# Kernel optimization log

Measured on AMD Instinct MI355X. Metric: run time of the kernel, lower is better.

Reference implementation:

```python
import jax, jax.numpy as jnp
import numpy as np

B, N = 1, 512
C_S, C_Z, C_H, H, PQ, PV = 384, 128, 16, 12, 4, 8
INF, EPS = 1e5, 1e-8
HW_INIT = 0.541324854612918  # softplus^{-1}(1), ipa_point_weights_init_


def _rotary(t, rot_dim, theta=10000.0):
    # lucidrains interleaved rotary over residue axis (axis 1); rotates first rot_dim channels
    n = t.shape[1]
    inv_freq = 1.0 / (theta ** (jnp.arange(0, rot_dim, 2, dtype=jnp.float32) / rot_dim))
    freqs = jnp.arange(n, dtype=jnp.float32)[:, None] * inv_freq  # [N, rot_dim//2]
    cos = jnp.cos(freqs)[None, :, None, :].astype(t.dtype)
    sin = jnp.sin(freqs)[None, :, None, :].astype(t.dtype)
    tr, tp = t[..., :rot_dim], t[..., rot_dim:]
    x1, x2 = tr[..., 0::2], tr[..., 1::2]
    tr = jnp.stack([x1 * cos - x2 * sin, x1 * sin + x2 * cos], axis=-1).reshape(tr.shape)
    return jnp.concatenate([tr, tp], axis=-1)


def _ipa(s, z, rot, trans, mask, Wq, bq, Wkv, bkv, Wqp, bqp, Wkvp, bkvp, Wb, bb,
         head_weights, Whid, bhid, Wpair, bpair, Wpts, bpts, Wpn, bpn):
    Bx, Nx = s.shape[0], s.shape[1]
    q = (s @ Wq + bq).reshape(Bx, Nx, H, C_H)
    kv = (s @ Wkv + bkv).reshape(Bx, Nx, H, 2 * C_H)
    k, v = kv[..., :C_H], kv[..., C_H:]

    def make_pts(x, npts):
        # channel layout: [x-block, y-block, z-block] -> [B,N,H*npts,3], then rigid apply R@p+t
        x = jnp.stack(jnp.split(x, 3, axis=-1), axis=-1)
        x = jnp.einsum('bnij,bnpj->bnpi', rot, x) + trans[:, :, None, :]
        return x.reshape(Bx, Nx, H, npts, 3)

    q_pts = make_pts(s @ Wqp + bqp, PQ)
    kv_pts = make_pts(s @ Wkvp + bkvp, PQ + PV)
    k_pts, v_pts = kv_pts[..., :PQ, :], kv_pts[..., PQ:, :]

    q = _rotary(q, C_H // 2)
    k = _rotary(k, C_H // 2)

    a = jnp.einsum('bihc,bjhc->bhij', q, k) * np.sqrt(1.0 / (3 * C_H))
    a = a + np.sqrt(1.0 / 3.0) * (jnp.einsum('bijc,ch->bhij', z, Wb) + bb[None, :, None, None])
    d2 = jnp.sum((q_pts[:, :, None] - k_pts[:, None]) ** 2, axis=-1)  # [B,Ni,Nj,H,PQ]
    hw = jax.nn.softplus(head_weights) * np.sqrt(1.0 / (3 * (PQ * 9.0 / 2)))
    a = a + jnp.transpose(-0.5 * jnp.sum(d2 * hw[None, None, None, :, None], axis=-1), (0, 3, 1, 2))
    sq_mask = INF * (mask[:, :, None] * mask[:, None, :] - 1.0)
    a = jax.nn.softmax(a + sq_mask[:, None], axis=-1)  # [B,H,N,N]

    o = jnp.einsum('bhij,bjhc->bihc', a, v).reshape(Bx, Nx, H * C_H)
    o_pt = jnp.einsum('bhij,bjhpx->bihpx', a, v_pts)  # [B,N,H,PV,3]
    o_pt = jnp.einsum('bnji,bnhpj->bnhpi', rot, o_pt - trans[:, :, None, None, :])  # invert_apply
    o_pt_norm = jnp.sqrt(jnp.sum(o_pt ** 2, axis=-1) + EPS).reshape(Bx, Nx, H * PV)
    o_pt = o_pt.reshape(Bx, Nx, H * PV, 3)
    pts_feat = jnp.concatenate([o_pt[..., 0], o_pt[..., 1], o_pt[..., 2]], axis=-1)
    o_pair = jnp.einsum('bhij,bijc->bihc', a, z).reshape(Bx, Nx, H * C_Z)

    s_out = ((o @ Whid + bhid) + (o_pair @ Wpair + bpair)
             + (pts_feat @ Wpts + bpts) + (o_pt_norm @ Wpn + bpn))
    return s_out, a


def setup_inputs() -> dict:
    key = jax.random.key(0)
    ks = jax.random.split(key, 16)
    f = lambda i, shape: jax.random.normal(ks[i], shape, dtype=jnp.float32)
    sc = 0.02
    rot, _ = jnp.linalg.qr(f(2, (B, N, 3, 3)))
    return {
        's': f(0, (B, N, C_S)),
        'z': f(1, (B, N, N, C_Z)),
        'rot': rot,
        'trans': f(3, (B, N, 3)),
        'mask': jnp.ones((B, N), jnp.float32),
        'Wq': f(4, (C_S, H * C_H)) * sc, 'bq': jnp.zeros((H * C_H,), jnp.float32),
        'Wkv': f(5, (C_S, 2 * H * C_H)) * sc, 'bkv': jnp.zeros((2 * H * C_H,), jnp.float32),
        'Wqp': f(6, (C_S, H * PQ * 3)) * sc, 'bqp': jnp.zeros((H * PQ * 3,), jnp.float32),
        'Wkvp': f(7, (C_S, H * (PQ + PV) * 3)) * sc, 'bkvp': jnp.zeros((H * (PQ + PV) * 3,), jnp.float32),
        'Wb': f(8, (C_Z, H)) * sc, 'bb': jnp.zeros((H,), jnp.float32),
        'head_weights': jnp.full((H,), HW_INIT, jnp.float32),
        'Whid': f(9, (H * C_H, C_S)) * sc, 'bhid': jnp.zeros((C_S,), jnp.float32),
        'Wpair': f(10, (H * C_Z, C_S)) * sc, 'bpair': jnp.zeros((C_S,), jnp.float32),
        'Wpts': f(11, (H * PV * 3, C_S)) * sc, 'bpts': jnp.zeros((C_S,), jnp.float32),
        'Wpn': f(12, (H * PV, C_S)) * sc, 'bpn': jnp.zeros((C_S,), jnp.float32),
    }


def reference(s, z, rot, trans, mask, Wq, bq, Wkv, bkv, Wqp, bqp, Wkvp, bkvp, Wb, bb,
              head_weights, Whid, bhid, Wpair, bpair, Wpts, bpts, Wpn, bpn):
    return _ipa(s, z, rot, trans, mask, Wq, bq, Wkv, bkv, Wqp, bqp, Wkvp, bkvp, Wb, bb,
                head_weights, Whid, bhid, Wpair, bpair, Wpts, bpts, Wpn, bpn)
```

## Files before the change

kernel.cpp:

```cpp
#include <hip/hip_runtime.h>
#include <hip/hip_bf16.h>
#include <cmath>

#define N 512
#define C_S 384
#define C_Z 128
#define C_H 16
#define H 12
#define PQ 4
#define PV 8

#define NJC 4
#define JCHUNK (N / NJC)
#define NPART 2016
#define NFEAT 2112
#define NRAW 1152
#define KSPLIT 11
#define KCHUNK 192

#define WS_Q    0
#define WS_K    (WS_Q + N*H*C_H)
#define WS_V    (WS_K + N*H*C_H)
#define WS_QP   (WS_V + N*H*C_H)
#define WS_KP   (WS_QP + N*H*PQ*3)
#define WS_VP   (WS_KP + N*H*PQ*3)
#define WS_PART (WS_VP + N*H*PV*3)
#define WS_FEAT (WS_PART + N*NJC*NPART)
#define WS_RAW  WS_PART
#define WS_KT   (WS_PART + 1200000)
#define WS_KPT  (WS_KT + 98304)
#define WS_WBT  (WS_KPT + 73728)
#define WS_FOUT WS_PART

__global__ __launch_bounds__(256) void k_gemm_proj(
    const float* __restrict__ s,
    const float* __restrict__ Wq,  const float* __restrict__ bq,
    const float* __restrict__ Wkv, const float* __restrict__ bkv,
    const float* __restrict__ Wqp, const float* __restrict__ bqp,
    const float* __restrict__ Wkvp,const float* __restrict__ bkvp,
    float* __restrict__ raw_out)
{
    const int m0 = blockIdx.x * 64;
    const int c0 = blockIdx.y * 64;
    const int t  = threadIdx.x;
    const int tc = t & 15;
    const int tm = t >> 4;

    __shared__ float st[64 * 33];
    __shared__ float wt[32 * 64];

    float acc[4][4];
#pragma unroll
    for (int u = 0; u < 4; ++u) {
        int col = c0 + tc*4 + u;
        const float* b; int cb;
        if (col < 192)      { b = bq;   cb = 0; }
        else if (col < 576) { b = bkv;  cb = 192; }
        else if (col < 720) { b = bqp;  cb = 576; }
        else                { b = bkvp; cb = 720; }
        float bv = b[col - cb];
#pragma unroll
        for (int r = 0; r < 4; ++r) acc[r][u] = bv;
    }

    for (int k0 = 0; k0 < C_S; k0 += 32) {
        __syncthreads();
        for (int e = t; e < 512; e += 256) {
            int row = e >> 3, kq = e & 7;
            float4 v = *(const float4*)&s[(size_t)(m0 + row)*C_S + k0 + kq*4];
            st[row*33 + kq*4 + 0] = v.x;
            st[row*33 + kq*4 + 1] = v.y;
            st[row*33 + kq*4 + 2] = v.z;
            st[row*33 + kq*4 + 3] = v.w;
        }
        for (int e = t; e < 512; e += 256) {
            int kk = e >> 4, c4 = e & 15;
            int col = c0 + c4*4;
            const float* W; int ncol, cb;
            if (col < 192)      { W = Wq;   ncol = 192; cb = 0; }
            else if (col < 576) { W = Wkv;  ncol = 384; cb = 192; }
            else if (col < 720) { W = Wqp;  ncol = 144; cb = 576; }
            else                { W = Wkvp; ncol = 432; cb = 720; }
            float4 v = *(const float4*)&W[(size_t)(k0 + kk)*ncol + (col - cb)];
            *(float4*)&wt[kk*64 + c4*4] = v;
        }
        __syncthreads();

#pragma unroll 8
        for (int kk = 0; kk < 32; ++kk) {
            float4 w = *(const float4*)&wt[kk*64 + tc*4];
            float sv[4];
#pragma unroll
            for (int r = 0; r < 4; ++r) sv[r] = st[(tm*4 + r)*33 + kk];
#pragma unroll
            for (int r = 0; r < 4; ++r) {
                acc[r][0] += sv[r] * w.x;
                acc[r][1] += sv[r] * w.y;
                acc[r][2] += sv[r] * w.z;
                acc[r][3] += sv[r] * w.w;
            }
        }
    }

#pragma unroll
    for (int r = 0; r < 4; ++r) {
        float4 o = make_float4(acc[r][0], acc[r][1], acc[r][2], acc[r][3]);
        *(float4*)&raw_out[(size_t)(m0 + tm*4 + r)*NRAW + c0 + tc*4] = o;
    }
}

__global__ __launch_bounds__(256) void k_post(
    const float* __restrict__ raw_in, const float* __restrict__ rot,
    const float* __restrict__ trans, const float* __restrict__ Wb,
    float* __restrict__ ws)
{
    const int n = blockIdx.x;
    const int t = threadIdx.x;
    __shared__ float raw[NRAW];

    for (int idx = t; idx < NRAW; idx += 256) raw[idx] = raw_in[(size_t)n*NRAW + idx];
    __syncthreads();

    if (n == 0) {
        for (int idx = t; idx < H*C_Z; idx += 256) {
            int h = idx >> 7, c = idx & 127;
            ws[WS_WBT + h*128 + c] = Wb[c*H + h];
        }
    }

    float R[9], T[3];
#pragma unroll
    for (int u = 0; u < 9; ++u) R[u] = rot[n*9 + u];
#pragma unroll
    for (int u = 0; u < 3; ++u) T[u] = trans[n*3 + u];

    float* q   = ws + WS_Q;
    float* v   = ws + WS_V;
    float* qp  = ws + WS_QP;
    float* vp  = ws + WS_VP;
    float* kT  = ws + WS_KT;
    float* kpT = ws + WS_KPT;

    for (int idx = t; idx < 1152; idx += 256) {
        if (idx < 192) {
            int h = idx >> 4, c = idx & 15;
            float val;
            if (c < 8) {
                int f = c >> 1;
                float x1 = raw[h*16 + 2*f];
                float x2 = raw[h*16 + 2*f + 1];
                float ang = (float)n * powf(10000.0f, -(float)(2*f) / 8.0f);
                float cs = cosf(ang), sn = sinf(ang);
                val = (c & 1) ? (x1*sn + x2*cs) : (x1*cs - x2*sn);
            } else {
                val = raw[h*16 + c];
            }
            q[n*192 + idx] = val;
        } else if (idx < 384) {
            int o = idx - 192, h = o >> 4, c = o & 15;
            float val;
            if (c < 8) {
                int f = c >> 1;
                float x1 = raw[192 + h*32 + 2*f];
                float x2 = raw[192 + h*32 + 2*f + 1];
                float ang = (float)n * powf(10000.0f, -(float)(2*f) / 8.0f);
                float cs = cosf(ang), sn = sinf(ang);
                val = (c & 1) ? (x1*sn + x2*cs) : (x1*cs - x2*sn);
            } else {
                val = raw[192 + h*32 + c];
            }
            kT[(size_t)o*N + n] = val;
        } else if (idx < 576) {
            int o = idx - 384, h = o >> 4, c = o & 15;
            v[n*192 + o] = raw[192 + h*32 + 16 + c];
        } else if (idx < 720) {
            int o = idx - 576;
            int hp = o / 3, ic = o - hp*3;
            float acc = T[ic];
#pragma unroll
            for (int j = 0; j < 3; ++j) acc += R[ic*3 + j] * raw[576 + j*48 + hp];
            qp[n*144 + o] = acc;
        } else {
            int o = idx - 720;
            int hp = o / 3, ic = o - hp*3;
            int h = hp / 12, p = hp - h*12;
            float acc = T[ic];
#pragma unroll
            for (int j = 0; j < 3; ++j) acc += R[ic*3 + j] * raw[720 + j*144 + hp];
            if (p < PQ) kpT[(size_t)(h*12 + p*3 + ic)*N + n] = acc;
            else        vp[n*(H*PV*3) + (h*PV + (p - PQ))*3 + ic] = acc;
        }
    }
}

__global__ __launch_bounds__(256) void k_logits(
    const float* __restrict__ ws, const float* __restrict__ z,
    const float* __restrict__ bb,
    const float* __restrict__ hwts, const float* __restrict__ mask,
    float* __restrict__ a_out)
{
    const int i  = blockIdx.x;
    const int j0 = blockIdx.y * 64;
    const int t  = threadIdx.x;
    const int j  = t & 63;
    const int jg = j0 + j;
    const int h0 = __builtin_amdgcn_readfirstlane(3 * (t >> 6));

    __shared__ float zt[64*132];

    const int srow = t >> 2;
    const int scq  = t & 3;
    float4 ra0, ra1, ra2, ra3, rb0, rb1, rb2, rb3;
    {
        const float* zbase = z + (((size_t)i*N) + j0)*C_Z;
        int e0 = t,       r0_ = e0 >> 4, c0_ = e0 & 15;
        int e1 = t + 256, r1_ = e1 >> 4, c1_ = e1 & 15;
        int e2 = t + 512, r2_ = e2 >> 4, c2_ = e2 & 15;
        int e3 = t + 768, r3_ = e3 >> 4, c3_ = e3 & 15;
        ra0 = *(const float4*)&zbase[(size_t)r0_*C_Z + c0_*4];
        ra1 = *(const float4*)&zbase[(size_t)r1_*C_Z + c1_*4];
        ra2 = *(const float4*)&zbase[(size_t)r2_*C_Z + c2_*4];
        ra3 = *(const float4*)&zbase[(size_t)r3_*C_Z + c3_*4];
        rb0 = *(const float4*)&zbase[(size_t)r0_*C_Z + 64 + c0_*4];
        rb1 = *(const float4*)&zbase[(size_t)r1_*C_Z + 64 + c1_*4];
        rb2 = *(const float4*)&zbase[(size_t)r2_*C_Z + 64 + c2_*4];
        rb3 = *(const float4*)&zbase[(size_t)r3_*C_Z + 64 + c3_*4];
    }

    const float* q   = ws + WS_Q  + (size_t)i*192;
    const float* qp  = ws + WS_QP + (size_t)i*144;
    const float* kT  = ws + WS_KT;
    const float* kpT = ws + WS_KPT;

    const float c1 = sqrtf(1.0f / 48.0f);
    const float c2 = sqrtf(1.0f / 3.0f);
    const float mterm = 100000.0f * (mask[i] * mask[jg] - 1.0f);

    float qkd[3];
#pragma unroll
    for (int u = 0; u < 3; ++u) {
        const int h = h0 + u;
        float qk = 0.0f;
#pragma unroll
        for (int c = 0; c < 16; ++c)
            qk += q[h*16 + c] * kT[(size_t)(h*16 + c)*N + jg];
        float d2s = 0.0f;
#pragma unroll
        for (int e = 0; e < 12; ++e) {
            float d = qp[h*12 + e] - kpT[(size_t)(h*12 + e)*N + jg];
            d2s += d*d;
        }
        float hw = log1pf(expf(hwts[h])) * sqrtf(1.0f / 54.0f);
        qkd[u] = c1*qk - 0.5f*hw*d2s + mterm + c2*bb[h];
    }

    {
        int e0 = t,       r0_ = e0 >> 4, c0_ = e0 & 15;
        int e1 = t + 256, r1_ = e1 >> 4, c1_ = e1 & 15;
        int e2 = t + 512, r2_ = e2 >> 4, c2_ = e2 & 15;
        int e3 = t + 768, r3_ = e3 >> 4, c3_ = e3 & 15;
        *(float4*)&zt[r0_*132 + c0_*4] = ra0;
        *(float4*)&zt[r1_*132 + c1_*4] = ra1;
        *(float4*)&zt[r2_*132 + c2_*4] = ra2;
        *(float4*)&zt[r3_*132 + c3_*4] = ra3;
    }
    __syncthreads();

    const float* w0 = ws + WS_WBT + (size_t)h0*128;
    float acc[3] = {0.0f, 0.0f, 0.0f};
#pragma unroll
    for (int c4 = 0; c4 < 16; ++c4) {
        float4 zv = *(const float4*)&zt[j*132 + c4*4];
        float4 b0 = *(const float4*)&w0[c4*4];
        float4 b1 = *(const float4*)&w0[128 + c4*4];
        float4 b2 = *(const float4*)&w0[256 + c4*4];
        acc[0] += zv.x*b0.x + zv.y*b0.y + zv.z*b0.z + zv.w*b0.w;
        acc[1] += zv.x*b1.x + zv.y*b1.y + zv.z*b1.z + zv.w*b1.w;
        acc[2] += zv.x*b2.x + zv.y*b2.y + zv.z*b2.z + zv.w*b2.w;
    }
    __syncthreads();

    {
        int e0 = t,       r0_ = e0 >> 4, c0_ = e0 & 15;
        int e1 = t + 256, r1_ = e1 >> 4, c1_ = e1 & 15;
        int e2 = t + 512, r2_ = e2 >> 4, c2_ = e2 & 15;
        int e3 = t + 768, r3_ = e3 >> 4, c3_ = e3 & 15;
        *(float4*)&zt[r0_*132 + 64 + c0_*4] = rb0;
        *(float4*)&zt[r1_*132 + 64 + c1_*4] = rb1;
        *(float4*)&zt[r2_*132 + 64 + c2_*4] = rb2;
        *(float4*)&zt[r3_*132 + 64 + c3_*4] = rb3;
    }
    __syncthreads();

#pragma unroll
    for (int c4 = 16; c4 < 32; ++c4) {
        float4 zv = *(const float4*)&zt[j*132 + c4*4];
        float4 b0 = *(const float4*)&w0[c4*4];
        float4 b1 = *(const float4*)&w0[128 + c4*4];
        float4 b2 = *(const float4*)&w0[256 + c4*4];
        acc[0] += zv.x*b0.x + zv.y*b0.y + zv.z*b0.z + zv.w*b0.w;
        acc[1] += zv.x*b1.x + zv.y*b1.y + zv.z*b1.z + zv.w*b1.w;
        acc[2] += zv.x*b2.x + zv.y*b2.y + zv.z*b2.z + zv.w*b2.w;
    }

#pragma unroll
    for (int u = 0; u < 3; ++u)
        a_out[((size_t)(h0 + u)*N + i)*N + jg] = qkd[u] + c2*acc[u];
}

__global__ __launch_bounds__(256) void k_softmax(float* __restrict__ a)
{
    const int row  = blockIdx.x*4 + (threadIdx.x >> 6);
    const int lane = threadIdx.x & 63;
    float* r = a + (size_t)row * N;

    float v[8];
    float m = -1e30f;
#pragma unroll
    for (int u = 0; u < 8; ++u) { v[u] = r[lane + 64*u]; m = fmaxf(m, v[u]); }
#pragma unroll
    for (int off = 32; off; off >>= 1) m = fmaxf(m, __shfl_xor(m, off));
    float ssum = 0.0f;
#pragma unroll
    for (int u = 0; u < 8; ++u) { v[u] = expf(v[u] - m); ssum += v[u]; }
#pragma unroll
    for (int off = 32; off; off >>= 1) ssum += __shfl_xor(ssum, off);
    float inv = 1.0f / ssum;
#pragma unroll
    for (int u = 0; u < 8; ++u) r[lane + 64*u] = v[u] * inv;
}

__global__ __launch_bounds__(256) void k_av(
    const float* __restrict__ a_full, const float* __restrict__ ws_ro,
    const float* __restrict__ z, float* __restrict__ ws)
{
    const int i  = blockIdx.x;
    const int jc = blockIdx.y;
    const int j0 = jc * JCHUNK;
    const int t  = threadIdx.x;

    __shared__ float a_s[H*JCHUNK];

    const float* v  = ws_ro + WS_V;
    const float* vp = ws_ro + WS_VP;
    float* part = ws + WS_PART + ((size_t)i*NJC + jc)*NPART;

    for (int e = t; e < H*JCHUNK; e += 256) {
        int h = e >> 7, jj = e & (JCHUNK-1);
        a_s[e] = a_full[((size_t)h*N + i)*N + j0 + jj];
    }
    __syncthreads();

    for (int idx = t; idx < 480; idx += 256) {
        float acc = 0.0f;
        if (idx < 192) {
            int h = idx >> 4;
            const float* vv = v + (size_t)j0*192 + idx;
            const float* ar = &a_s[h*JCHUNK];
#pragma unroll 8
            for (int jj = 0; jj < JCHUNK; ++jj) acc += ar[jj] * vv[(size_t)jj*192];
        } else {
            int o = idx - 192;
            int h = (o/3) >> 3;
            const float* vv = vp + (size_t)j0*288 + o;
            const float* ar = &a_s[h*JCHUNK];
#pragma unroll 8
            for (int jj = 0; jj < JCHUNK; ++jj) acc += ar[jj] * vv[(size_t)jj*288];
        }
        part[idx] = acc;
    }

    {
        const int c  = t & 127;
        const int hb = t >> 7;
        float acc[6];
#pragma unroll
        for (int u = 0; u < 6; ++u) acc[u] = 0.0f;
        const float* zi = z + ((size_t)i*N + j0)*C_Z + c;
        for (int jj = 0; jj < JCHUNK; jj += 8) {
            float zr[8];
#pragma unroll
            for (int r = 0; r < 8; ++r) zr[r] = zi[(size_t)(jj+r)*C_Z];
            float4 av0[6], av1[6];
#pragma unroll
            for (int u = 0; u < 6; ++u) {
                av0[u] = *(const float4*)&a_s[(hb + 2*u)*JCHUNK + jj];
                av1[u] = *(const float4*)&a_s[(hb + 2*u)*JCHUNK + jj + 4];
            }
#pragma unroll
            for (int u = 0; u < 6; ++u) {
                acc[u] += av0[u].x*zr[0] + av0[u].y*zr[1] + av0[u].z*zr[2] + av0[u].w*zr[3];
                acc[u] += av1[u].x*zr[4] + av1[u].y*zr[5] + av1[u].z*zr[6] + av1[u].w*zr[7];
            }
        }
#pragma unroll
        for (int u = 0; u < 6; ++u) part[480 + (hb + 2*u)*C_Z + c] = acc[u];
    }
}

__global__ __launch_bounds__(256) void k_feat(
    const float* __restrict__ rot, const float* __restrict__ trans,
    float* __restrict__ ws)
{
    const int i = blockIdx.x;
    const int t = threadIdx.x;

    __shared__ float vec[NPART];

    const float* part = ws + WS_PART + (size_t)i*NJC*NPART;
    float* feat = ws + WS_FEAT + (size_t)i*NFEAT;

    for (int e = t; e < NPART; e += 256) {
        float acc = 0.0f;
#pragma unroll
        for (int jc = 0; jc < NJC; ++jc) acc += part[(size_t)jc*NPART + e];
        vec[e] = acc;
    }
    __syncthreads();

    for (int e = t; e < NPART; e += 256) {
        if (e < 192)       feat[e] = vec[e];
        else if (e >= 480) feat[192 + (e - 480)] = vec[e];
    }

    if (t < H*PV) {
        const int hp = t;
        float T0 = trans[i*3+0], T1 = trans[i*3+1], T2 = trans[i*3+2];
        float px = vec[192 + hp*3 + 0] - T0;
        float py = vec[192 + hp*3 + 1] - T1;
        float pz = vec[192 + hp*3 + 2] - T2;
        const float* R = rot + i*9;
        float ox = R[0]*px + R[3]*py + R[6]*pz;
        float oy = R[1]*px + R[4]*py + R[7]*pz;
        float oz = R[2]*px + R[5]*py + R[8]*pz;
        feat[1728 + hp]       = ox;
        feat[1728 + 96 + hp]  = oy;
        feat[1728 + 192 + hp] = oz;
        feat[2016 + hp] = sqrtf(ox*ox + oy*oy + oz*oz + 1e-8f);
    }
}

__global__ __launch_bounds__(256) void k_final_part(
    const float* __restrict__ ws,
    const float* __restrict__ Whid, const float* __restrict__ Wpair,
    const float* __restrict__ Wpts, const float* __restrict__ Wpn,
    float* __restrict__ fout)
{
    const int m0 = blockIdx.x * 64;
    const int c0 = blockIdx.y * 64;
    const int kc = blockIdx.z;
    const int t  = threadIdx.x;
    const int tc = t & 15;
    const int tm = t >> 4;

    __shared__ float ft[64 * 33];
    __shared__ float wt[32 * 64];

    const float* feat = ws + WS_FEAT;

    float acc[4][4];
#pragma unroll
    for (int r = 0; r < 4; ++r)
#pragma unroll
        for (int u = 0; u < 4; ++u) acc[r][u] = 0.0f;

    const int kbase = kc * KCHUNK;
    for (int k0 = kbase; k0 < kbase + KCHUNK; k0 += 32) {
        const float* W; int r0;
        if (k0 < 192)       { W = Whid;  r0 = k0; }
        else if (k0 < 1728) { W = Wpair; r0 = k0 - 192; }
        else if (k0 < 2016) { W = Wpts;  r0 = k0 - 1728; }
        else                { W = Wpn;   r0 = k0 - 2016; }

        __syncthreads();
        for (int e = t; e < 512; e += 256) {
            int row = e >> 3, kq = e & 7;
            float4 v = *(const float4*)&feat[(size_t)(m0 + row)*NFEAT + k0 + kq*4];
            ft[row*33 + kq*4 + 0] = v.x;
            ft[row*33 + kq*4 + 1] = v.y;
            ft[row*33 + kq*4 + 2] = v.z;
            ft[row*33 + kq*4 + 3] = v.w;
        }
        for (int e = t; e < 512; e += 256) {
            int kk = e >> 4, c4 = e & 15;
            float4 v = *(const float4*)&W[(size_t)(r0 + kk)*C_S + c0 + c4*4];
            *(float4*)&wt[kk*64 + c4*4] = v;
        }
        __syncthreads();

#pragma unroll 8
        for (int kk = 0; kk < 32; ++kk) {
            float4 w = *(const float4*)&wt[kk*64 + tc*4];
            float sv[4];
#pragma unroll
            for (int r = 0; r < 4; ++r) sv[r] = ft[(tm*4 + r)*33 + kk];
#pragma unroll
            for (int r = 0; r < 4; ++r) {
                acc[r][0] += sv[r] * w.x;
                acc[r][1] += sv[r] * w.y;
                acc[r][2] += sv[r] * w.z;
                acc[r][3] += sv[r] * w.w;
            }
        }
    }

#pragma unroll
    for (int r = 0; r < 4; ++r) {
        float4 o = make_float4(acc[r][0], acc[r][1], acc[r][2], acc[r][3]);
        *(float4*)&fout[((size_t)kc*N + m0 + tm*4 + r)*C_S + c0 + tc*4] = o;
    }
}

__global__ __launch_bounds__(256) void k_red(
    const float* __restrict__ fout,
    const float* __restrict__ bhid, const float* __restrict__ bpair,
    const float* __restrict__ bpts, const float* __restrict__ bpn,
    float* __restrict__ s_out)
{
    const int idx = blockIdx.x * 256 + threadIdx.x;
    const int c = idx % C_S;
    float acc = bhid[c] + bpair[c] + bpts[c] + bpn[c];
#pragma unroll
    for (int kc = 0; kc < KSPLIT; ++kc)
        acc += fout[(size_t)kc*N*C_S + idx];
    s_out[idx] = acc;
}

extern "C" void kernel_launch(void* const* d_in, const int* in_sizes, int n_in,
                              void* d_out, int out_size, void* d_ws, size_t ws_size,
                              hipStream_t stream) {
    const float* s     = (const float*)d_in[0];
    const float* z     = (const float*)d_in[1];
    const float* rot   = (const float*)d_in[2];
    const float* trans = (const float*)d_in[3];
    const float* mask  = (const float*)d_in[4];
    const float* Wq    = (const float*)d_in[5];
    const float* bq    = (const float*)d_in[6];
    const float* Wkv   = (const float*)d_in[7];
    const float* bkv   = (const float*)d_in[8];
    const float* Wqp   = (const float*)d_in[9];
    const float* bqp   = (const float*)d_in[10];
    const float* Wkvp  = (const float*)d_in[11];
    const float* bkvp  = (const float*)d_in[12];
    const float* Wb    = (const float*)d_in[13];
    const float* bb    = (const float*)d_in[14];
    const float* hwts  = (const float*)d_in[15];
    const float* Whid  = (const float*)d_in[16];
    const float* bhid  = (const float*)d_in[17];
    const float* Wpair = (const float*)d_in[18];
    const float* bpair = (const float*)d_in[19];
    const float* Wpts  = (const float*)d_in[20];
    const float* bpts  = (const float*)d_in[21];
    const float* Wpn   = (const float*)d_in[22];
    const float* bpn   = (const float*)d_in[23];

    float* out   = (float*)d_out;
    float* s_out = out;
    float* a_out = out + N*C_S;
    float* ws    = (float*)d_ws;

    k_gemm_proj<<<dim3(8, 18), 256, 0, stream>>>(s, Wq, bq, Wkv, bkv, Wqp, bqp,
                                                 Wkvp, bkvp, ws + WS_RAW);
    k_post<<<N, 256, 0, stream>>>(ws + WS_RAW, rot, trans, Wb, ws);
    k_logits<<<dim3(N, 8), 256, 0, stream>>>(ws, z, bb, hwts, mask, a_out);
    k_softmax<<<(H*N)/4, 256, 0, stream>>>(a_out);
    k_av<<<dim3(N, NJC), 256, 0, stream>>>(a_out, ws, z, ws);
    k_feat<<<N, 256, 0, stream>>>(rot, trans, ws);
    k_final_part<<<dim3(8, 6, KSPLIT), 256, 0, stream>>>(ws, Whid, Wpair, Wpts,
                                                         Wpn, ws + WS_FOUT);
    k_red<<<(N*C_S)/256, 256, 0, stream>>>(ws + WS_FOUT, bhid, bpair, bpts, bpn,
                                           s_out);
}
```

Baseline: 164.1 us.

## Repack K/Kpt into float4-interleaved layout and transpose V/Vpt for vectorized loads

The projection kernel now writes K and key points in a layout that interleaves groups of four channels per residue, and writes V and value points transposed as channel-major. The logits kernel reads K and key points as float4 per residue instead of 28 scalar strided loads. The AV kernel walks each channel's V row contiguously, using float4 loads from both global memory and shared memory. The goal is fewer memory instructions and more contiguous access, at the cost of scattered scalar stores when writing the transposed layouts in the producer kernel.

```diff
diff --git a/kernel.cpp b/kernel.cpp
--- a/kernel.cpp
+++ b/kernel.cpp
@@ -134,12 +134,12 @@
 #pragma unroll
     for (int u = 0; u < 3; ++u) T[u] = trans[n*3 + u];
 
-    float* q   = ws + WS_Q;
-    float* v   = ws + WS_V;
-    float* qp  = ws + WS_QP;
-    float* vp  = ws + WS_VP;
-    float* kT  = ws + WS_KT;
-    float* kpT = ws + WS_KPT;
+    float* q    = ws + WS_Q;
+    float* vT   = ws + WS_V;
+    float* qp   = ws + WS_QP;
+    float* vpT  = ws + WS_VP;
+    float* kT4  = ws + WS_KT;
+    float* kpT4 = ws + WS_KPT;
 
     for (int idx = t; idx < 1152; idx += 256) {
         if (idx < 192) {
@@ -169,10 +169,10 @@
             } else {
                 val = raw[192 + h*32 + c];
             }
-            kT[(size_t)o*N + n] = val;
+            kT4[((size_t)(o >> 2)*N + n)*4 + (o & 3)] = val;
         } else if (idx < 576) {
             int o = idx - 384, h = o >> 4, c = o & 15;
-            v[n*192 + o] = raw[192 + h*32 + 16 + c];
+            vT[(size_t)o*N + n] = raw[192 + h*32 + 16 + c];
         } else if (idx < 720) {
             int o = idx - 576;
             int hp = o / 3, ic = o - hp*3;
@@ -187,8 +187,12 @@
             float acc = T[ic];
 #pragma unroll
             for (int j = 0; j < 3; ++j) acc += R[ic*3 + j] * raw[720 + j*144 + hp];
-            if (p < PQ) kpT[(size_t)(h*12 + p*3 + ic)*N + n] = acc;
-            else        vp[n*(H*PV*3) + (h*PV + (p - PQ))*3 + ic] = acc;
+            if (p < PQ) {
+                int e = h*12 + p*3 + ic;
+                kpT4[((size_t)(e >> 2)*N + n)*4 + (e & 3)] = acc;
+            } else {
+                vpT[(size_t)((h*PV + (p - PQ))*3 + ic)*N + n] = acc;
+            }
         }
     }
 }
@@ -208,8 +212,6 @@
 
     __shared__ float zt[64*132];
 
-    const int srow = t >> 2;
-    const int scq  = t & 3;
     float4 ra0, ra1, ra2, ra3, rb0, rb1, rb2, rb3;
     {
         const float* zbase = z + (((size_t)i*N) + j0)*C_Z;
@@ -227,10 +229,10 @@
         rb3 = *(const float4*)&zbase[(size_t)r3_*C_Z + 64 + c3_*4];
     }
 
-    const float* q   = ws + WS_Q  + (size_t)i*192;
-    const float* qp  = ws + WS_QP + (size_t)i*144;
-    const float* kT  = ws + WS_KT;
-    const float* kpT = ws + WS_KPT;
+    const float* q    = ws + WS_Q  + (size_t)i*192;
+    const float* qp   = ws + WS_QP + (size_t)i*144;
+    const float* kT4  = ws + WS_KT;
+    const float* kpT4 = ws + WS_KPT;
 
     const float c1 = sqrtf(1.0f / 48.0f);
     const float c2 = sqrtf(1.0f / 3.0f);
@@ -242,13 +244,20 @@
         const int h = h0 + u;
         float qk = 0.0f;
 #pragma unroll
-        for (int c = 0; c < 16; ++c)
-            qk += q[h*16 + c] * kT[(size_t)(h*16 + c)*N + jg];
+        for (int cq = 0; cq < 4; ++cq) {
+            float4 kv = *(const float4*)&kT4[((size_t)(h*4 + cq)*N + jg)*4];
+            qk += q[h*16 + cq*4 + 0]*kv.x + q[h*16 + cq*4 + 1]*kv.y
+                + q[h*16 + cq*4 + 2]*kv.z + q[h*16 + cq*4 + 3]*kv.w;
+        }
         float d2s = 0.0f;
 #pragma unroll
-        for (int e = 0; e < 12; ++e) {
-            float d = qp[h*12 + e] - kpT[(size_t)(h*12 + e)*N + jg];
-            d2s += d*d;
+        for (int eq = 0; eq < 3; ++eq) {
+            float4 pv = *(const float4*)&kpT4[((size_t)(h*3 + eq)*N + jg)*4];
+            float d;
+            d = qp[h*12 + eq*4 + 0] - pv.x; d2s += d*d;
+            d = qp[h*12 + eq*4 + 1] - pv.y; d2s += d*d;
+            d = qp[h*12 + eq*4 + 2] - pv.z; d2s += d*d;
+            d = qp[h*12 + eq*4 + 3] - pv.w; d2s += d*d;
         }
         float hw = log1pf(expf(hwts[h])) * sqrtf(1.0f / 54.0f);
         qkd[u] = c1*qk - 0.5f*hw*d2s + mterm + c2*bb[h];
@@ -341,8 +350,8 @@
 
     __shared__ float a_s[H*JCHUNK];
 
-    const float* v  = ws_ro + WS_V;
-    const float* vp = ws_ro + WS_VP;
+    const float* vT  = ws_ro + WS_V;
+    const float* vpT = ws_ro + WS_VP;
     float* part = ws + WS_PART + ((size_t)i*NJC + jc)*NPART;
 
     for (int e = t; e < H*JCHUNK; e += 256) {
@@ -353,19 +362,15 @@
 
     for (int idx = t; idx < 480; idx += 256) {
         float acc = 0.0f;
-        if (idx < 192) {
-            int h = idx >> 4;
-            const float* vv = v + (size_t)j0*192 + idx;
-            const float* ar = &a_s[h*JCHUNK];
+        const float* src; int h;
+        if (idx < 192) { src = vT + (size_t)idx*N + j0; h = idx >> 4; }
+        else { int o = idx - 192; src = vpT + (size_t)o*N + j0; h = (o/3) >> 3; }
+        const float* ar = &a_s[h*JCHUNK];
 #pragma unroll 8
-            for (int jj = 0; jj < JCHUNK; ++jj) acc += ar[jj] * vv[(size_t)jj*192];
-        } else {
-            int o = idx - 192;
-            int h = (o/3) >> 3;
-            const float* vv = vp + (size_t)j0*288 + o;
-            const float* ar = &a_s[h*JCHUNK];
-#pragma unroll 8
-            for (int jj = 0; jj < JCHUNK; ++jj) acc += ar[jj] * vv[(size_t)jj*288];
+        for (int jj = 0; jj < JCHUNK; jj += 4) {
+            float4 vv = *(const float4*)&src[jj];
+            float4 aa = *(const float4*)&ar[jj];
+            acc += vv.x*aa.x + vv.y*aa.y + vv.z*aa.z + vv.w*aa.w;
         }
         part[idx] = acc;
     }
```

Measured after the change: 192.5 us. 17.3% more time.
